# Kernel tuning notes

Measured on AMD Instinct MI355X. Metric: run time of the kernel, lower is better.

Reference implementation:

```python
import jax, jax.numpy as jnp
import numpy as np

B, S = 128, 128
AH, VH, TH = 64, 64, 128  # audio/vision/text LSTM hidden sizes
FUSED = (AH + 1) * (VH + 1) * (TH + 1)  # 545025
PF = 128  # post_fusion_dim


def setup_inputs() -> dict:
    key = jax.random.key(0)
    ks = jax.random.split(key, 6)
    return {
        "audio_h": jax.random.normal(ks[0], (B, S, AH), jnp.float32),
        "vision_h": jax.random.normal(ks[1], (B, S, VH), jnp.float32),
        "text_h": jax.random.normal(ks[2], (B, S, TH), jnp.float32),
        "W1": jax.random.normal(ks[3], (PF, FUSED), jnp.float32) * 0.001,
        "b1": jnp.zeros((PF,), jnp.float32),
        "W2": jax.random.normal(ks[4], (PF, PF), jnp.float32) * 0.05,
        "b2": jnp.zeros((PF,), jnp.float32),
        "W3": jax.random.normal(ks[5], (1, PF), jnp.float32) * 0.05,
        "b3": jnp.zeros((1,), jnp.float32),
    }


def reference(audio_h, vision_h, text_h, W1, b1, W2, b2, W3, b3):
    b, s = audio_h.shape[0], audio_h.shape[1]
    ones = jnp.ones((b, s, 1), audio_h.dtype)
    a = jnp.concatenate([ones, audio_h], axis=2)   # [B,S,AH+1]
    v = jnp.concatenate([ones, vision_h], axis=2)  # [B,S,VH+1]
    t = jnp.concatenate([ones, text_h], axis=2)    # [B,S,TH+1]
    # sum_t outer(a_t, v_t, t_t): one fused contraction over the time axis
    fusion = jnp.einsum('bsa,bsv,bsw->bavw', a, v, t)  # [B,AH+1,VH+1,TH+1]
    fusion = fusion.reshape(b, -1)                      # matches torch view order (a,v,t)
    # T2FN low-rank regularizer scale
    tmp = jnp.sqrt(jnp.asarray(AH * VH * TH / max(AH, VH, TH), jnp.float32))
    # post-fusion MLP (dropout p=0 -> identity)
    y1 = jax.nn.relu(fusion @ W1.T + b1)
    y2 = jax.nn.relu(y1 @ W2.T + b2)
    out = y2 @ W3.T + b3  # [B,1]
    out = jax.nn.sigmoid(out) * 6.0 - 3.0  # output_range=6, output_shift=-3
    norm = jnp.linalg.norm(fusion, axis=1)  # [B]
    reg_loss = jnp.mean(tmp * norm)
    return (out, reg_loss)
```

## Files before the change

kernel.cpp:

```cpp
#include <hip/hip_runtime.h>
#include <math.h>

#define BB 128
#define SS 128
#define AE 65
#define VE 65
#define TE 129
#define PFD 128
#define FUSED 545025UL
#define FUSEDI 545025
#define VSTRIDE 136
#define APLANE 8840
#define FPP 574976UL
#define FPPI 574976
#define KSP 512
#define NBLK 1123
#define NST 8

typedef _Float16 half8 __attribute__((ext_vector_type(8)));
typedef float f32x16 __attribute__((ext_vector_type(16)));

__device__ __forceinline__ void gll16(const void* g, void* l) {
  __builtin_amdgcn_global_load_lds((const __attribute__((address_space(1))) void*)g,
                                   (__attribute__((address_space(3))) void*)l, 16, 0, 0);
}

__global__ __launch_bounds__(256) void k_initf(_Float16* __restrict__ Fh,
                                               float* __restrict__ y1pre,
                                               float* __restrict__ normsq,
                                               float* __restrict__ Flast) {
  const int b = blockIdx.x;
  const int tid = threadIdx.x;
  _Float16* base = Fh + (size_t)b * FPP;
  for (int i = tid; i < 29575; i += 256) {
    const int a = i / 455, r = i - a * 455;
    const int v = r / 7, e = r - v * 7;
    base[a * APLANE + v * VSTRIDE + 129 + e] = (_Float16)0.f;
  }
  for (int i = tid; i < 376; i += 256) base[574600 + i] = (_Float16)0.f;
  if (tid < PFD) y1pre[b * PFD + tid] = 0.f;
  if (tid == 128) normsq[b] = 0.f;
  if (tid == 129) Flast[b] = 0.f;
}

__global__ __launch_bounds__(256) void k_core(
    const float* __restrict__ audio, const float* __restrict__ vision,
    const float* __restrict__ text, _Float16* __restrict__ Fh,
    float* __restrict__ normsq)
{
  const int b  = blockIdx.x;
  const int gy = blockIdx.y;
  const int gz = blockIdx.z;
  const int tid = threadIdx.x;
  const int wv = tid >> 6, ln = tid & 63;
  const int lr = ln & 31, hb = ln >> 5;

  __shared__ float    sVt[64][132];
  __shared__ float    sAc[8][132];
  __shared__ _Float16 sTh[64][136];
  __shared__ _Float16 sTl[64][136];

  {
    const float* vb = vision + (size_t)b * SS * 64;
#pragma unroll
    for (int r = 0; r < 32; ++r) {
      const int e = tid + 256 * r;
      sVt[e & 63][e >> 6] = vb[e];
    }
    const float* ab = audio + (size_t)b * SS * 64 + 8 * gy;
#pragma unroll
    for (int r = 0; r < 4; ++r) {
      const int e = tid + 256 * r;
      sAc[e & 7][e >> 3] = ab[(e >> 3) * 64 + (e & 7)];
    }
    const int wbase = 64 * gz;
    const float* tb = text + (size_t)b * SS * 128;
#pragma unroll
    for (int r = 0; r < 32; ++r) {
      const int e = tid + 256 * r;
      const int s = e >> 6, wl = e & 63;
      const int w = wbase + wl;
      const float val = (w == 0) ? 1.f : tb[s * 128 + w - 1];
      const _Float16 th = (_Float16)val;
      sTh[wl][s] = th;
      sTl[wl][s] = (_Float16)((val - (float)th) * 2048.f);
    }
  }
  __syncthreads();

  float ss = 0.f;
  for (int r = 0; r < 4; ++r) {
    const int rt = 4 * wv + r;
    const int j  = rt >> 1, vh = rt & 1;
    const int v0m = 32 * vh;

    f32x16 accA = {}, acclA = {}, accB = {}, acclB = {};
#pragma unroll
    for (int ks = 0; ks < 8; ++ks) {
      const int s0 = 16 * ks + 8 * hb;
      const float4 x0 = *(const float4*)&sVt[v0m + lr][s0];
      const float4 x1 = *(const float4*)&sVt[v0m + lr][s0 + 4];
      const float4 a0 = *(const float4*)&sAc[j][s0];
      const float4 a1 = *(const float4*)&sAc[j][s0 + 4];
      const float pp[8] = {a0.x * x0.x, a0.y * x0.y, a0.z * x0.z, a0.w * x0.w,
                           a1.x * x1.x, a1.y * x1.y, a1.z * x1.z, a1.w * x1.w};
      half8 afh, afl;
#pragma unroll
      for (int e = 0; e < 8; ++e) {
        const _Float16 h = (_Float16)pp[e];
        afh[e] = h;
        afl[e] = (_Float16)((pp[e] - (float)h) * 2048.f);
      }
      const half8 bqh0 = *(const half8*)&sTh[lr][s0];
      const half8 bql0 = *(const half8*)&sTl[lr][s0];
      const half8 bqh1 = *(const half8*)&sTh[32 + lr][s0];
      const half8 bql1 = *(const half8*)&sTl[32 + lr][s0];
      accA  = __builtin_amdgcn_mfma_f32_32x32x16_f16(afh, bqh0, accA,  0, 0, 0);
      acclA = __builtin_amdgcn_mfma_f32_32x32x16_f16(afl, bqh0, acclA, 0, 0, 0);
      acclA = __builtin_amdgcn_mfma_f32_32x32x16_f16(afh, bql0, acclA, 0, 0, 0);
      accB  = __builtin_amdgcn_mfma_f32_32x32x16_f16(afh, bqh1, accB,  0, 0, 0);
      acclB = __builtin_amdgcn_mfma_f32_32x32x16_f16(afl, bqh1, acclB, 0, 0, 0);
      acclB = __builtin_amdgcn_mfma_f32_32x32x16_f16(afh, bql1, acclB, 0, 0, 0);
    }

    const int a = 1 + 8 * gy + j;
    _Float16* Fb = Fh + (size_t)b * FPP + (size_t)a * APLANE;
    const int wg0 = 64 * gz + lr;
    const int wg1 = 64 * gz + 32 + lr;
#pragma unroll
    for (int reg = 0; reg < 16; ++reg) {
      const int crow = (reg & 3) + 8 * (reg >> 2) + 4 * hb;
      const int v = 1 + 32 * vh + crow;
      const float fA = accA[reg] + acclA[reg] * (1.f / 2048.f);
      const float fB = accB[reg] + acclB[reg] * (1.f / 2048.f);
      ss += fA * fA + fB * fB;
      Fb[(size_t)v * VSTRIDE + wg0] = (_Float16)fA;
      Fb[(size_t)v * VSTRIDE + wg1] = (_Float16)fB;
    }
  }

#pragma unroll
  for (int off = 32; off > 0; off >>= 1) ss += __shfl_down(ss, off);
  if (ln == 0) atomicAdd(&normsq[b], ss);
}

__global__ __launch_bounds__(256) void k_planes(
    const float* __restrict__ audio, const float* __restrict__ vision,
    const float* __restrict__ text, _Float16* __restrict__ Fh,
    float* __restrict__ Flast, float* __restrict__ normsq)
{
  const int b = blockIdx.x;
  const int which = blockIdx.y;
  const int tid = threadIdx.x;
  const int tw = tid & 15, tv = tid >> 4;
  __shared__ __align__(16) char smem[28800];

  float ss = 0.f;

  if (which == 0) {
    float (*sv)[80]  = (float(*)[80])smem;
    float (*st)[144] = (float(*)[144])(smem + 10240);
    float acc[5][9];
#pragma unroll
    for (int i = 0; i < 5; ++i)
#pragma unroll
      for (int j = 0; j < 9; ++j) acc[i][j] = 0.f;

    for (int c = 0; c < 4; ++c) {
      const int s0 = 32 * c;
      __syncthreads();
      const float* vbase = &vision[((size_t)(b * SS + s0)) * 64];
#pragma unroll
      for (int r = 0; r < 8; ++r) {
        const int e = tid + 256 * r;
        sv[e >> 6][(e & 63) + 1] = vbase[e];
      }
      const float* tbase = &text[((size_t)(b * SS + s0)) * 128];
#pragma unroll
      for (int r = 0; r < 16; ++r) {
        const int e = tid + 256 * r;
        st[e >> 7][(e & 127) + 1] = tbase[e];
      }
      if (tid < 32) { sv[tid][0] = 1.f; st[tid][0] = 1.f; }
      __syncthreads();
      for (int s = 0; s < 32; ++s) {
        float vr[5], tr[9];
#pragma unroll
        for (int i = 0; i < 5; ++i) {
          const int vx = tv + 16 * i;
          vr[i] = (vx < VE) ? sv[s][vx] : 0.f;
        }
#pragma unroll
        for (int j = 0; j < 9; ++j) {
          const int wx = tw + 16 * j;
          tr[j] = (wx < TE) ? st[s][wx] : 0.f;
        }
#pragma unroll
        for (int i = 0; i < 5; ++i)
#pragma unroll
          for (int j = 0; j < 9; ++j) acc[i][j] += vr[i] * tr[j];
      }
    }
    _Float16* Fb = Fh + (size_t)b * FPP;
#pragma unroll
    for (int i = 0; i < 5; ++i) {
      const int v = tv + 16 * i;
      if (v < VE) {
#pragma unroll
        for (int j = 0; j < 9; ++j) {
          const int w = tw + 16 * j;
          if (w < TE) {
            const float m = acc[i][j];
            Fb[(size_t)v * VSTRIDE + w] = (_Float16)m;
            ss += m * m;
          }
        }
      }
    }
  } else if (which == 1) {
    float (*sa)[64]  = (float(*)[64])smem;
    float (*st)[144] = (float(*)[144])(smem + 10240);
    float acc[4][9];
#pragma unroll
    for (int i = 0; i < 4; ++i)
#pragma unroll
      for (int j = 0; j < 9; ++j) acc[i][j] = 0.f;

    for (int c = 0; c < 4; ++c) {
      const int s0 = 32 * c;
      __syncthreads();
      const float* abase = &audio[((size_t)(b * SS + s0)) * 64];
#pragma unroll
      for (int r = 0; r < 8; ++r) {
        const int e = tid + 256 * r;
        sa[e >> 6][e & 63] = abase[e];
      }
      const float* tbase = &text[((size_t)(b * SS + s0)) * 128];
#pragma unroll
      for (int r = 0; r < 16; ++r) {
        const int e = tid + 256 * r;
        st[e >> 7][(e & 127) + 1] = tbase[e];
      }
      if (tid < 32) st[tid][0] = 1.f;
      __syncthreads();
      for (int s = 0; s < 32; ++s) {
        float ar[4], tr[9];
#pragma unroll
        for (int i = 0; i < 4; ++i) ar[i] = sa[s][tv + 16 * i];
#pragma unroll
        for (int j = 0; j < 9; ++j) {
          const int wx = tw + 16 * j;
          tr[j] = (wx < TE) ? st[s][wx] : 0.f;
        }
#pragma unroll
        for (int i = 0; i < 4; ++i)
#pragma unroll
          for (int j = 0; j < 9; ++j) acc[i][j] += ar[i] * tr[j];
      }
    }
#pragma unroll
    for (int i = 0; i < 4; ++i) {
      const int a = 1 + tv + 16 * i;
      _Float16* Fb = Fh + (size_t)b * FPP + (size_t)a * APLANE;
#pragma unroll
      for (int j = 0; j < 9; ++j) {
        const int w = tw + 16 * j;
        if (w < TE) {
          const float m = acc[i][j];
          Fb[w] = (_Float16)m;
          ss += m * m;
        }
      }
    }
  } else {
    float (*sa)[64] = (float(*)[64])smem;
    float (*sv)[64] = (float(*)[64])(smem + 10240);
    float* swt = (float*)(smem + 10240 + 8192);
    float acc[4][4];
#pragma unroll
    for (int i = 0; i < 4; ++i)
#pragma unroll
      for (int j = 0; j < 4; ++j) acc[i][j] = 0.f;

    for (int c = 0; c < 4; ++c) {
      const int s0 = 32 * c;
      __syncthreads();
      const float* abase = &audio[((size_t)(b * SS + s0)) * 64];
      const float* vbase = &vision[((size_t)(b * SS + s0)) * 64];
#pragma unroll
      for (int r = 0; r < 8; ++r) {
        const int e = tid + 256 * r;
        sa[e >> 6][e & 63] = abase[e];
        sv[e >> 6][e & 63] = vbase[e];
      }
      if (tid < 32) swt[tid] = text[((size_t)(b * SS + s0 + tid)) * 128 + 127];
      __syncthreads();
      for (int s = 0; s < 32; ++s) {
        const float t = swt[s];
        float ar[4], vr[4];
#pragma unroll
        for (int i = 0; i < 4; ++i) ar[i] = sa[s][tv + 16 * i] * t;
#pragma unroll
        for (int j = 0; j < 4; ++j) vr[j] = sv[s][tw + 16 * j];
#pragma unroll
        for (int i = 0; i < 4; ++i)
#pragma unroll
          for (int j = 0; j < 4; ++j) acc[i][j] += ar[i] * vr[j];
      }
    }
#pragma unroll
    for (int i = 0; i < 4; ++i) {
      const int a = 1 + tv + 16 * i;
      _Float16* Fb = Fh + (size_t)b * FPP + (size_t)a * APLANE;
#pragma unroll
      for (int j = 0; j < 4; ++j) {
        const int v = 1 + tw + 16 * j;
        float m = acc[i][j];
        ss += m * m;
        if (a == 64 && v == 64) { Flast[b] = m; m = 0.f; }
        Fb[(size_t)v * VSTRIDE + 128] = (_Float16)m;
      }
    }
  }

#pragma unroll
  for (int off = 32; off > 0; off >>= 1) ss += __shfl_down(ss, off);
  if ((tid & 63) == 0) atomicAdd(&normsq[b], ss);
}

__global__ __launch_bounds__(256) void k_gemm(
    const float* __restrict__ W1, const _Float16* __restrict__ Fh,
    float* __restrict__ parts)
{
  __shared__ _Float16 sB[2][8192];

  const int tid = threadIdx.x;
  const int wv = tid >> 6, ln = tid & 63;
  const int lb = ln & 31, hb = ln >> 5;
  const int p  = (wv << 5) + lb;
  const int kp0 = blockIdx.x * KSP;

  int wtr[4], kot[4];
#pragma unroll
  for (int j = 0; j < 4; ++j) {
    const int kpl = kp0 + 16 * j + (hb << 3);
    const int a = kpl / APLANE;
    const int rem = kpl - a * APLANE;
    const int v = rem / VSTRIDE;
    wtr[j] = rem - v * VSTRIDE;
    kot[j] = a * 8385 + v * 129 + wtr[j];
  }
  const float* wrow = W1 + (size_t)p * FUSED;

  const int brow = (wv << 5) + (ln >> 3);
  const int sslot = (ln & 7) ^ ((ln >> 3) & 7);
  const _Float16* FhB = Fh + (size_t)brow * FPP + kp0 + (sslot << 3);

  f32x16 acc0 = {}, acc1 = {}, acc2 = {}, acc3 = {};
  float4 xa[8];

#define LOADA                                                              \
  {                                                                        \
    _Pragma("unroll")                                                      \
    for (int j = 0; j < 4; ++j) {                                          \
      const int kc = (kot[j] <= 545017) ? kot[j] : 545008;                 \
      __builtin_memcpy(&xa[2 * j], wrow + kc, 16);                         \
      __builtin_memcpy(&xa[2 * j + 1], wrow + kc + 4, 16);                 \
      wtr[j] += 64;                                                        \
      if (wtr[j] >= VSTRIDE) { wtr[j] -= VSTRIDE; kot[j] += 57; }          \
      else kot[j] += 64;                                                   \
    }                                                                      \
  }

#define STAGEB(BUF, KOFF)                                                  \
  {                                                                        \
    _Pragma("unroll")                                                      \
    for (int n = 0; n < 4; ++n) {                                          \
      gll16(FhB + (size_t)(n << 3) * FPP + (KOFF),                         \
            (char*)&sB[BUF][0] + (((wv << 5) + (n << 3)) << 7));           \
    }                                                                      \
  }

  LOADA
  STAGEB(0, 0)
  __syncthreads();

  int buf = 0;
  for (int t = 0; t < NST; ++t) {
    half8 af[4];
#pragma unroll
    for (int j = 0; j < 4; ++j) {
      af[j][0] = (_Float16)xa[2 * j].x;     af[j][1] = (_Float16)xa[2 * j].y;
      af[j][2] = (_Float16)xa[2 * j].z;     af[j][3] = (_Float16)xa[2 * j].w;
      af[j][4] = (_Float16)xa[2 * j + 1].x; af[j][5] = (_Float16)xa[2 * j + 1].y;
      af[j][6] = (_Float16)xa[2 * j + 1].z; af[j][7] = (_Float16)xa[2 * j + 1].w;
    }
    if (t + 1 < NST) {
      LOADA
      STAGEB(buf ^ 1, (t + 1) * 64)
    }
    const _Float16* sBb = &sB[buf][0];
#pragma unroll
    for (int j = 0; j < 4; ++j) {
      const int slot = ((j << 1) + hb) ^ (lb & 7);
      const char* bbase = (const char*)sBb + (lb << 7) + (slot << 4);
      const half8 b0 = *(const half8*)(bbase);
      const half8 b1 = *(const half8*)(bbase + 4096);
      const half8 b2 = *(const half8*)(bbase + 8192);
      const half8 b3 = *(const half8*)(bbase + 12288);
      acc0 = __builtin_amdgcn_mfma_f32_32x32x16_f16(af[j], b0, acc0, 0, 0, 0);
      acc1 = __builtin_amdgcn_mfma_f32_32x32x16_f16(af[j], b1, acc1, 0, 0, 0);
      acc2 = __builtin_amdgcn_mfma_f32_32x32x16_f16(af[j], b2, acc2, 0, 0, 0);
      acc3 = __builtin_amdgcn_mfma_f32_32x32x16_f16(af[j], b3, acc3, 0, 0, 0);
    }
    __syncthreads();
    buf ^= 1;
  }
#undef LOADA
#undef STAGEB

  f32x16* o = (f32x16*)(parts + ((size_t)blockIdx.x * 256 + tid) * 64);
  o[0] = acc0; o[1] = acc1; o[2] = acc2; o[3] = acc3;
}

__global__ __launch_bounds__(256) void k_red(const float* __restrict__ parts,
                                             float* __restrict__ y1pre)
{
  const int tid = threadIdx.x;
  const int T = blockIdx.x * 4 + (tid >> 6);
  const int R = tid & 63;
  float s = 0.f;
  for (int sl = blockIdx.y; sl < NBLK; sl += 16)
    s += parts[(size_t)sl * 16384 + T * 64 + R];
  const int wv2 = T >> 6, hb2 = (T >> 5) & 1, lb2 = T & 31;
  const int q = R >> 4, rg = R & 15;
  const int b = q * 32 + lb2;
  const int pp = wv2 * 32 + (rg & 3) + 8 * (rg >> 2) + 4 * hb2;
  atomicAdd(&y1pre[b * PFD + pp], s);
}

__global__ __launch_bounds__(128) void k_final(
    const float* __restrict__ y1pre, const float* __restrict__ b1,
    const float* __restrict__ W2, const float* __restrict__ b2,
    const float* __restrict__ W3, const float* __restrict__ b3,
    const float* __restrict__ W1, const float* __restrict__ Flast,
    const float* __restrict__ normsq, float* __restrict__ out)
{
  const int b = blockIdx.x, p = threadIdx.x;
  __shared__ float y1[PFD];
  __shared__ float red[PFD];
  const float extra = W1[(size_t)p * FUSED + (FUSED - 1)] * Flast[b];
  y1[p] = fmaxf(y1pre[(size_t)b * PFD + p] + extra + b1[p], 0.f);
  __syncthreads();
  float s = b2[p];
  for (int k = 0; k < PFD; ++k) s += y1[k] * W2[p * PFD + k];
  const float y2 = fmaxf(s, 0.f);
  red[p] = y2 * W3[p];
  __syncthreads();
  for (int off = 64; off > 0; off >>= 1) {
    if (p < off) red[p] += red[p + off];
    __syncthreads();
  }
  if (p == 0) {
    const float x = red[0] + b3[0];
    out[b] = 6.f / (1.f + expf(-x)) - 3.f;
  }
  if (b == 0) {
    __syncthreads();
    red[p] = sqrtf(normsq[p]);
    __syncthreads();
    for (int off = 64; off > 0; off >>= 1) {
      if (p < off) red[p] += red[p + off];
      __syncthreads();
    }
    if (p == 0) out[BB] = 64.f * red[0] / (float)BB;
  }
}

extern "C" void kernel_launch(void* const* d_in, const int* in_sizes, int n_in,
                              void* d_out, int out_size, void* d_ws, size_t ws_size,
                              hipStream_t stream) {
  const float* audio  = (const float*)d_in[0];
  const float* vision = (const float*)d_in[1];
  const float* text   = (const float*)d_in[2];
  const float* W1     = (const float*)d_in[3];
  const float* b1     = (const float*)d_in[4];
  const float* W2     = (const float*)d_in[5];
  const float* b2     = (const float*)d_in[6];
  const float* W3     = (const float*)d_in[7];
  const float* b3     = (const float*)d_in[8];
  float* out = (float*)d_out;

  float* y1pre  = (float*)d_ws;
  float* normsq = y1pre + BB * PFD;
  float* Flast  = normsq + BB;
  _Float16* Fh  = (_Float16*)((char*)d_ws + 131072);
  float* parts  = (float*)((char*)d_ws + 147324928);

  k_initf<<<BB, 256, 0, stream>>>(Fh, y1pre, normsq, Flast);

  k_core<<<dim3(BB, 8, 2), 256, 0, stream>>>(audio, vision, text, Fh, normsq);
  k_planes<<<dim3(BB, 3), 256, 0, stream>>>(audio, vision, text, Fh, Flast, normsq);

  k_gemm<<<NBLK, 256, 0, stream>>>(W1, Fh, parts);
  k_red<<<dim3(64, 16), 256, 0, stream>>>(parts, y1pre);

  k_final<<<BB, PFD, 0, stream>>>(y1pre, b1, W2, b2, W3, b3, W1, Flast, normsq, out);
}
```

Before: 350.5 us.

## Coalesce W1 loads via LDS staging in GEMM and split fusion tile loop

The main GEMM kernel used to have each lane read 32-byte chunks from its own W1 row at scattered offsets. It now has 16 lanes cover 64 contiguous floats of a row and loads 8 rows per thread, converts them to fp16, and writes them into a swizzled per-wave LDS tile. The MFMA A fragments are then read back from that tile, which gives coalesced global reads of W1 at the cost of extra LDS traffic and capacity. The fusion-plane kernel is also restructured to produce one 32-wide output tile per iteration instead of two. That halves accumulator register pressure but doubles the loop count.

```diff
diff --git a/kernel.cpp b/kernel.cpp
--- a/kernel.cpp
+++ b/kernel.cpp
@@ -17,6 +17,7 @@
 #define NBLK 1123
 #define NST 8
 
+typedef _Float16 half4 __attribute__((ext_vector_type(4)));
 typedef _Float16 half8 __attribute__((ext_vector_type(8)));
 typedef float f32x16 __attribute__((ext_vector_type(16)));
 
@@ -89,12 +90,14 @@
   __syncthreads();
 
   float ss = 0.f;
-  for (int r = 0; r < 4; ++r) {
-    const int rt = 4 * wv + r;
+  for (int i = 0; i < 8; ++i) {
+    const int u  = 8 * wv + i;
+    const int rt = u >> 1, wt = u & 1;
     const int j  = rt >> 1, vh = rt & 1;
     const int v0m = 32 * vh;
-
-    f32x16 accA = {}, acclA = {}, accB = {}, acclB = {};
+    const int wl0 = 32 * wt;
+
+    f32x16 acc = {}, accl = {};
 #pragma unroll
     for (int ks = 0; ks < 8; ++ks) {
       const int s0 = 16 * ks + 8 * hb;
@@ -111,31 +114,23 @@
         afh[e] = h;
         afl[e] = (_Float16)((pp[e] - (float)h) * 2048.f);
       }
-      const half8 bqh0 = *(const half8*)&sTh[lr][s0];
-      const half8 bql0 = *(const half8*)&sTl[lr][s0];
-      const half8 bqh1 = *(const half8*)&sTh[32 + lr][s0];
-      const half8 bql1 = *(const half8*)&sTl[32 + lr][s0];
-      accA  = __builtin_amdgcn_mfma_f32_32x32x16_f16(afh, bqh0, accA,  0, 0, 0);
-      acclA = __builtin_amdgcn_mfma_f32_32x32x16_f16(afl, bqh0, acclA, 0, 0, 0);
-      acclA = __builtin_amdgcn_mfma_f32_32x32x16_f16(afh, bql0, acclA, 0, 0, 0);
-      accB  = __builtin_amdgcn_mfma_f32_32x32x16_f16(afh, bqh1, accB,  0, 0, 0);
-      acclB = __builtin_amdgcn_mfma_f32_32x32x16_f16(afl, bqh1, acclB, 0, 0, 0);
-      acclB = __builtin_amdgcn_mfma_f32_32x32x16_f16(afh, bql1, acclB, 0, 0, 0);
+      const half8 bqh = *(const half8*)&sTh[wl0 + lr][s0];
+      const half8 bql = *(const half8*)&sTl[wl0 + lr][s0];
+      acc  = __builtin_amdgcn_mfma_f32_32x32x16_f16(afh, bqh, acc,  0, 0, 0);
+      accl = __builtin_amdgcn_mfma_f32_32x32x16_f16(afl, bqh, accl, 0, 0, 0);
+      accl = __builtin_amdgcn_mfma_f32_32x32x16_f16(afh, bql, accl, 0, 0, 0);
     }
 
     const int a = 1 + 8 * gy + j;
     _Float16* Fb = Fh + (size_t)b * FPP + (size_t)a * APLANE;
-    const int wg0 = 64 * gz + lr;
-    const int wg1 = 64 * gz + 32 + lr;
+    const int wg = 64 * gz + wl0 + lr;
 #pragma unroll
     for (int reg = 0; reg < 16; ++reg) {
       const int crow = (reg & 3) + 8 * (reg >> 2) + 4 * hb;
       const int v = 1 + 32 * vh + crow;
-      const float fA = accA[reg] + acclA[reg] * (1.f / 2048.f);
-      const float fB = accB[reg] + acclB[reg] * (1.f / 2048.f);
-      ss += fA * fA + fB * fB;
-      Fb[(size_t)v * VSTRIDE + wg0] = (_Float16)fA;
-      Fb[(size_t)v * VSTRIDE + wg1] = (_Float16)fB;
+      const float f = acc[reg] + accl[reg] * (1.f / 2048.f);
+      ss += f * f;
+      Fb[(size_t)v * VSTRIDE + wg] = (_Float16)f;
     }
   }
 
@@ -333,24 +328,24 @@
     float* __restrict__ parts)
 {
   __shared__ _Float16 sB[2][8192];
+  __shared__ _Float16 sA[4][2048];
 
   const int tid = threadIdx.x;
   const int wv = tid >> 6, ln = tid & 63;
   const int lb = ln & 31, hb = ln >> 5;
-  const int p  = (wv << 5) + lb;
   const int kp0 = blockIdx.x * KSP;
 
-  int wtr[4], kot[4];
-#pragma unroll
-  for (int j = 0; j < 4; ++j) {
-    const int kpl = kp0 + 16 * j + (hb << 3);
+  const int loff = (ln & 15) << 2;
+  int wtr, kot;
+  {
+    const int kpl = kp0 + loff;
     const int a = kpl / APLANE;
     const int rem = kpl - a * APLANE;
     const int v = rem / VSTRIDE;
-    wtr[j] = rem - v * VSTRIDE;
-    kot[j] = a * 8385 + v * 129 + wtr[j];
-  }
-  const float* wrow = W1 + (size_t)p * FUSED;
+    wtr = rem - v * VSTRIDE;
+    kot = a * 8385 + v * 129 + wtr;
+  }
+  const float* wbase = W1 + (size_t)((wv << 5) + (ln >> 4)) * FUSED;
 
   const int brow = (wv << 5) + (ln >> 3);
   const int sslot = (ln & 7) ^ ((ln >> 3) & 7);
@@ -361,14 +356,24 @@
 
 #define LOADA                                                              \
   {                                                                        \
+    const int kc = (kot <= 545021) ? kot : 545021;                         \
     _Pragma("unroll")                                                      \
-    for (int j = 0; j < 4; ++j) {                                          \
-      const int kc = (kot[j] <= 545017) ? kot[j] : 545008;                 \
-      __builtin_memcpy(&xa[2 * j], wrow + kc, 16);                         \
-      __builtin_memcpy(&xa[2 * j + 1], wrow + kc + 4, 16);                 \
-      wtr[j] += 64;                                                        \
-      if (wtr[j] >= VSTRIDE) { wtr[j] -= VSTRIDE; kot[j] += 57; }          \
-      else kot[j] += 64;                                                   \
+    for (int n = 0; n < 8; ++n)                                            \
+      __builtin_memcpy(&xa[n], wbase + (size_t)(4 * n) * FUSED + kc, 16);  \
+    wtr += 64;                                                             \
+    if (wtr >= VSTRIDE) { wtr -= VSTRIDE; kot += 57; } else kot += 64;     \
+  }
+
+#define WRITEA                                                             \
+  {                                                                        \
+    _Pragma("unroll")                                                      \
+    for (int n = 0; n < 8; ++n) {                                          \
+      const int Rl = 4 * n + (ln >> 4);                                    \
+      const int sp = (((ln & 15) >> 1) ^ (Rl & 7));                        \
+      half4 h;                                                             \
+      h[0] = (_Float16)xa[n].x; h[1] = (_Float16)xa[n].y;                  \
+      h[2] = (_Float16)xa[n].z; h[3] = (_Float16)xa[n].w;                  \
+      *(half4*)((char*)&sA[wv][0] + (Rl << 7) + (sp << 4) + ((ln & 1) << 3)) = h; \
     }                                                                      \
   }
 
@@ -387,36 +392,32 @@
 
   int buf = 0;
   for (int t = 0; t < NST; ++t) {
-    half8 af[4];
-#pragma unroll
-    for (int j = 0; j < 4; ++j) {
-      af[j][0] = (_Float16)xa[2 * j].x;     af[j][1] = (_Float16)xa[2 * j].y;
-      af[j][2] = (_Float16)xa[2 * j].z;     af[j][3] = (_Float16)xa[2 * j].w;
-      af[j][4] = (_Float16)xa[2 * j + 1].x; af[j][5] = (_Float16)xa[2 * j + 1].y;
-      af[j][6] = (_Float16)xa[2 * j + 1].z; af[j][7] = (_Float16)xa[2 * j + 1].w;
-    }
+    WRITEA
     if (t + 1 < NST) {
       LOADA
       STAGEB(buf ^ 1, (t + 1) * 64)
     }
     const _Float16* sBb = &sB[buf][0];
+    const char* sAw = (const char*)&sA[wv][0] + (lb << 7);
 #pragma unroll
     for (int j = 0; j < 4; ++j) {
+      const half8 af = *(const half8*)(sAw + ((((j << 1) + hb) ^ (lb & 7)) << 4));
       const int slot = ((j << 1) + hb) ^ (lb & 7);
       const char* bbase = (const char*)sBb + (lb << 7) + (slot << 4);
       const half8 b0 = *(const half8*)(bbase);
       const half8 b1 = *(const half8*)(bbase + 4096);
       const half8 b2 = *(const half8*)(bbase + 8192);
       const half8 b3 = *(const half8*)(bbase + 12288);
-      acc0 = __builtin_amdgcn_mfma_f32_32x32x16_f16(af[j], b0, acc0, 0, 0, 0);
-      acc1 = __builtin_amdgcn_mfma_f32_32x32x16_f16(af[j], b1, acc1, 0, 0, 0);
-      acc2 = __builtin_amdgcn_mfma_f32_32x32x16_f16(af[j], b2, acc2, 0, 0, 0);
-      acc3 = __builtin_amdgcn_mfma_f32_32x32x16_f16(af[j], b3, acc3, 0, 0, 0);
+      acc0 = __builtin_amdgcn_mfma_f32_32x32x16_f16(af, b0, acc0, 0, 0, 0);
+      acc1 = __builtin_amdgcn_mfma_f32_32x32x16_f16(af, b1, acc1, 0, 0, 0);
+      acc2 = __builtin_amdgcn_mfma_f32_32x32x16_f16(af, b2, acc2, 0, 0, 0);
+      acc3 = __builtin_amdgcn_mfma_f32_32x32x16_f16(af, b3, acc3, 0, 0, 0);
     }
     __syncthreads();
     buf ^= 1;
   }
 #undef LOADA
+#undef WRITEA
 #undef STAGEB
 
   f32x16* o = (f32x16*)(parts + ((size_t)blockIdx.x * 256 + tid) * 64);
```

Result: faster. 314.2 us (median of 3 runs) (-10.3%).
